# Kernel tuning notes

Hardware: AMD Instinct MI355X
Metric: run time of the kernel (lower is better)

The kernel has to match this reference:

```python
import jax, jax.numpy as jnp
import numpy as np

SCALE = 0.125  # (dim // heads) ** -0.5 = (256 // 4) ** -0.5


def setup_inputs() -> dict:
    key = jax.random.key(0)
    k1, k2, k3, k4, k5 = jax.random.split(key, 5)
    dim, red = 256, 4
    c = dim // red  # 64
    B, H, W = 4, 64, 64
    x = jax.random.normal(k1, (B, dim, H, W), dtype=jnp.float32)
    qkv_w = jax.random.normal(k2, (3 * c, dim), dtype=jnp.float32) * 0.02
    qkv_b = jax.random.normal(k3, (3 * c,), dtype=jnp.float32) * 0.02
    proj_w = jax.random.normal(k4, (dim, c), dtype=jnp.float32) * 0.02
    proj_b = jax.random.normal(k5, (dim,), dtype=jnp.float32) * 0.02
    return {"x": x, "qkv_w": qkv_w, "qkv_b": qkv_b, "proj_w": proj_w, "proj_b": proj_b}


def reference(x, qkv_w, qkv_b, proj_w, proj_b):
    B, C, H, W = x.shape
    # 1x1 conv == channel matmul
    qkv = jnp.einsum('bchw,oc->bohw', x, qkv_w) + qkv_b[None, :, None, None]
    c = qkv.shape[1] // 3
    qkv = qkv.reshape(B, 3 * c, H * W)
    q, k, v = qkv[:, :c], qkv[:, c:2 * c], qkv[:, 2 * c:]  # [B, c, HW]
    # attn[b, n, m] = sum_c q[b,c,n] * k[b,c,m] * scale
    attn = jnp.einsum('bcn,bcm->bnm', q, k) * SCALE
    attn = jax.nn.softmax(attn, axis=-1)  # [B, HW, HW]
    # out[b, c, n] = sum_m v[b,c,m] * attn[b,n,m]   (v @ attn^T)
    out = jnp.einsum('bcm,bnm->bcn', v, attn).reshape(B, c, H, W)
    # proj 1x1 conv back to dim
    return jnp.einsum('bchw,oc->bohw', out, proj_w) + proj_b[None, :, None, None]
```

## Files before the change

kernel.cpp:

```cpp
#include <hip/hip_runtime.h>
#include <hip/hip_bf16.h>


#define N_TOK 4096
#define CDIM  64
#define DIM   256
#define NBAT  4

typedef __attribute__((ext_vector_type(8)))  short          short8;
typedef __attribute__((ext_vector_type(8)))  unsigned short ushort8_t;
typedef __attribute__((ext_vector_type(4)))  unsigned short ushort4_t;
typedef __attribute__((ext_vector_type(4)))  unsigned int   uint4_t;
typedef __attribute__((ext_vector_type(4)))  float          float4_t;
typedef __attribute__((ext_vector_type(16))) float          float16_t;

#if __has_builtin(__builtin_amdgcn_exp2f)
#define QSC  0.18033688011112042f
#define PEXP(x) __builtin_amdgcn_exp2f(x)
#else
#define QSC  0.125f
#define PEXP(x) __expf(x)
#endif

__device__ __forceinline__ unsigned short f2bf(float f) {
  unsigned int u = __builtin_bit_cast(unsigned int, f);
  u += 0x7fffu + ((u >> 16) & 1u);
  return (unsigned short)(u >> 16);
}

__device__ __forceinline__ unsigned int pkcv(float a, float b) {
  __hip_bfloat162 h = __float22bfloat162_rn(make_float2(a, b));
  unsigned int r; __builtin_memcpy(&r, &h, 4); return r;
}

__device__ __forceinline__ short8 ld8(const unsigned short* p) {
  return __builtin_bit_cast(short8, *(const ushort8_t*)p);
}

__device__ __forceinline__ short8 pack8f(float4_t a, float4_t b) {
  uint4_t u;
  u[0] = pkcv(a[0], a[1]); u[1] = pkcv(a[2], a[3]);
  u[2] = pkcv(b[0], b[1]); u[3] = pkcv(b[2], b[3]);
  return __builtin_bit_cast(short8, u);
}

__device__ __forceinline__ float16_t z16() {
  float16_t r;
#pragma unroll
  for (int i = 0; i < 16; ++i) r[i] = 0.0f;
  return r;
}

typedef __attribute__((address_space(1))) const void* gvp;
typedef __attribute__((address_space(3))) void*       lvp;
__device__ __forceinline__ void dma16(const unsigned short* g, unsigned short* l) {
  __builtin_amdgcn_global_load_lds((gvp)g, (lvp)l, 16, 0, 0);
}

#define MFMA(a, b, c) __builtin_amdgcn_mfma_f32_32x32x16_bf16((a), (b), (c), 0, 0, 0)

#define QOFF  0
#define KOFF  1048576
#define VOFF  2097152
#define WQOFF 3145728
#define BSOFF 3194880

__global__ void k_prep(const float* __restrict__ qw, const float* __restrict__ qb,
                       unsigned short* __restrict__ wqs, float* __restrict__ bs)
{
  const int g = blockIdx.x * 256 + threadIdx.x;
  {
    const int lane = g & 63, grp = g >> 6;
    const int w6 = grp >> 4, kk = grp & 15;
    const int o = w6 * 32 + (lane & 31);
    const int c = kk * 16 + (lane >> 5) * 8;
    const float sc = (o < 64) ? QSC : 1.0f;
    const float* src = qw + o * 256 + c;
    ushort8_t u;
#pragma unroll
    for (int j = 0; j < 8; ++j) u[j] = f2bf(src[j] * sc);
    *(ushort8_t*)(wqs + g * 8) = u;
  }
  if (g < 48) {
    float4_t f = *(const float4_t*)(qb + g * 4);
    float4_t o;
#pragma unroll
    for (int j = 0; j < 4; ++j) o[j] = f[j] * ((g * 4 + j) < 64 ? QSC : 1.0f);
    *(float4_t*)(bs + g * 4) = o;
  }
}

#define RS 132

__global__ __launch_bounds__(384, 2) void k_qkv(
    const float* __restrict__ x, const unsigned short* __restrict__ wqs,
    const float* __restrict__ bs, unsigned short* __restrict__ Qf,
    unsigned short* __restrict__ Kf, unsigned short* __restrict__ Vf)
{
  __shared__ unsigned int Xl[64 * RS];
  const int id = blockIdx.x;
  const int b  = (id >> 1) & 3;
  const int nt = (id & 1) | ((id >> 3) << 1);
  const int t  = threadIdx.x;
  const int n0g = nt * 64;

  if (t < 256) {
    const int n0  = (t & 15) * 4;
    const int cpb = t >> 4;
#pragma unroll
    for (int p = 0; p < 8; ++p) {
      const int cp = cpb + 16 * p, c = cp * 2;
      const float* xb = x + (((size_t)(b * DIM + c)) << 12) + n0g + n0;
      float4_t a = *(const float4_t*)xb;
      float4_t d = *(const float4_t*)(xb + 4096);
#pragma unroll
      for (int j = 0; j < 4; ++j)
        Xl[(n0 + j) * RS + cp] = pkcv(a[j], d[j]);
    }
  }
  __syncthreads();

  const int w = t >> 6, lane = t & 63, l31 = lane & 31, lh = lane >> 5;
  const unsigned short* wrow = wqs + ((w * 16) << 9) + lane * 8;
  const unsigned int*   xr0  = &Xl[l31 * RS + lh * 4];
  const unsigned int*   xr1  = &Xl[(32 + l31) * RS + lh * 4];

  float16_t a0 = z16(), a1 = z16();
  if (w < 4) {
#pragma unroll
    for (int kk = 0; kk < 16; ++kk) {
      short8 wf = ld8(wrow + (kk << 9));
      short8 x0 = __builtin_bit_cast(short8, *(const uint4_t*)(xr0 + kk * 8));
      short8 x1 = __builtin_bit_cast(short8, *(const uint4_t*)(xr1 + kk * 8));
      a0 = MFMA(wf, x0, a0);
      a1 = MFMA(wf, x1, a1);
    }
  } else {
#pragma unroll
    for (int kk = 0; kk < 16; ++kk) {
      short8 wf = ld8(wrow + (kk << 9));
      short8 x0 = __builtin_bit_cast(short8, *(const uint4_t*)(xr0 + kk * 8));
      short8 x1 = __builtin_bit_cast(short8, *(const uint4_t*)(xr1 + kk * 8));
      a0 = MFMA(x0, wf, a0);
      a1 = MFMA(x1, wf, a1);
    }
  }

  if (w < 4) {
    unsigned short* dst = (w < 2) ? Qf : Kf;
    const int w2 = w & 1;
#pragma unroll
    for (int sub = 0; sub < 2; ++sub) {
      const float16_t& aa = sub ? a1 : a0;
      const int ch = nt * 2 + sub;
#pragma unroll
      for (int p = 0; p < 4; ++p) {
        const int o = w * 32 + p * 8 + lh * 4;
        float4_t bv = *(const float4_t*)(bs + o);
        ushort4_t pk4;
#pragma unroll
        for (int q = 0; q < 4; ++q) pk4[q] = f2bf(aa[p * 4 + q] + bv[q]);
        const int kkt = w2 * 2 + (p >> 1);
        *(ushort4_t*)(dst + ((((b * 128 + ch) * 4 + kkt) << 9)
                             + (l31 + 32 * (p & 1)) * 8 + lh * 4)) = pk4;
      }
    }
  } else {
    const int ct = w - 4;
    const float bvs = bs[128 + ct * 32 + l31];
#pragma unroll
    for (int sub = 0; sub < 2; ++sub) {
      const float16_t& aa = sub ? a1 : a0;
      const int ch = nt * 2 + sub;
#pragma unroll
      for (int ks = 0; ks < 2; ++ks) {
        ushort8_t pk8;
#pragma unroll
        for (int j = 0; j < 8; ++j) pk8[j] = f2bf(aa[ks * 8 + j] + bvs);
        *(ushort8_t*)(Vf + ((((b * 128 + ch) * 4 + ct * 2 + ks) << 9)
                            + lane * 8)) = pk8;
      }
    }
  }
}

#define OS   68
#define OLS  72
#define NACC (64 * OS + 64)

__global__ __launch_bounds__(512, 1) void k_attn(
    const unsigned short* __restrict__ Qf, const unsigned short* __restrict__ Kf,
    const unsigned short* __restrict__ Vf, const float* __restrict__ pw,
    const float* __restrict__ pb, float* __restrict__ out)
{
  __shared__ __align__(16) unsigned short KV[2][2][16384];
  __shared__ float Oacc[NACC];
  __shared__ __align__(16) unsigned short Ol[64 * OLS];

  const int id = blockIdx.x;
  const int b  = (id >> 1) & 3;
  const int nt = (id & 1) | ((id >> 3) << 1);
  const int t  = threadIdx.x;
  const int wv = t >> 6, lane = t & 63, l31 = lane & 31, lh = lane >> 5;
  const int mq = wv >> 1, nsub = wv & 1;

  for (int i = t; i < NACC; i += 512) Oacc[i] = 0.0f;

  const int kvsel = wv >> 2;
  const int wq2   = (wv & 3) * 2;
  const unsigned short* sg = ((kvsel == 0) ? Kf : Vf)
                             + (((size_t)(b * 128 + wq2)) << 11) + lane * 8;

  short8 qf[4];
#pragma unroll
  for (int kk = 0; kk < 4; ++kk)
    qf[kk] = ld8(Qf + (((b * 128 + nt * 2 + nsub) * 4 + kk) << 9) + lane * 8);

#pragma unroll
  for (int c2 = 0; c2 < 2; ++c2)
#pragma unroll
    for (int kk = 0; kk < 4; ++kk)
      dma16(sg + (c2 << 11) + (kk << 9),
            &KV[0][kvsel][((wq2 + c2) << 11) + (kk << 9)]);

  float16_t oc0 = z16(), oc1 = z16();
  float den = 0.0f;

  __syncthreads();

  for (int t4 = 0; t4 < 16; ++t4) {
    const int cur = t4 & 1;

    if (t4 < 15) {
      const unsigned short* g = sg + (((size_t)(t4 + 1)) << 14);
#pragma unroll
      for (int c2 = 0; c2 < 2; ++c2)
#pragma unroll
        for (int kk = 0; kk < 4; ++kk)
          dma16(g + (c2 << 11) + (kk << 9),
                &KV[cur ^ 1][kvsel][((wq2 + c2) << 11) + (kk << 9)]);
    }

#pragma unroll
    for (int cc = 0; cc < 2; ++cc) {
      const int ch = mq * 2 + cc;
      const unsigned short* kl = &KV[cur][0][ch << 11];
      const unsigned short* vl = &KV[cur][1][ch << 11];

      short8 kf0 = ld8(kl + lane * 8);
      short8 kf1 = ld8(kl + 512 + lane * 8);
      short8 kf2 = ld8(kl + 1024 + lane * 8);
      short8 kf3 = ld8(kl + 1536 + lane * 8);

      float16_t s = z16();
      s = MFMA(kf0, qf[0], s);
      s = MFMA(kf1, qf[1], s);
      s = MFMA(kf2, qf[2], s);
      s = MFMA(kf3, qf[3], s);

      float p[16];
#pragma unroll
      for (int e = 0; e < 16; ++e) p[e] = PEXP(s[e]);
      {
        float d0 = (p[0] + p[1]) + (p[2] + p[3]);
        float d1 = (p[4] + p[5]) + (p[6] + p[7]);
        float d2 = (p[8] + p[9]) + (p[10] + p[11]);
        float d3 = (p[12] + p[13]) + (p[14] + p[15]);
        den += (d0 + d1) + (d2 + d3);
      }

      uint4_t w0, w1;
#pragma unroll
      for (int j = 0; j < 4; ++j) {
        w0[j] = pkcv(p[2 * j], p[2 * j + 1]);
        w1[j] = pkcv(p[8 + 2 * j], p[9 + 2 * j]);
      }
      short8 pf0 = __builtin_bit_cast(short8, w0);
      short8 pf1 = __builtin_bit_cast(short8, w1);

      short8 vf0 = ld8(vl + lane * 8);
      short8 vf1 = ld8(vl + 512 + lane * 8);
      short8 vf2 = ld8(vl + 1024 + lane * 8);
      short8 vf3 = ld8(vl + 1536 + lane * 8);

      oc0 = MFMA(pf0, vf0, oc0);
      oc0 = MFMA(pf1, vf1, oc0);
      oc1 = MFMA(pf0, vf2, oc1);
      oc1 = MFMA(pf1, vf3, oc1);
    }

    __syncthreads();
  }

  den += __shfl_xor(den, 32);

#pragma unroll
  for (int ct = 0; ct < 2; ++ct) {
    const float16_t& oa = ct ? oc1 : oc0;
    const int cc = ct * 32 + l31;
#pragma unroll
    for (int e = 0; e < 16; ++e) {
      const int nr = nsub * 32 + (e & 3) + 8 * (e >> 2) + 4 * lh;
      atomicAdd(&Oacc[nr * OS + cc], oa[e]);
    }
  }
  if (lane < 32) atomicAdd(&Oacc[64 * OS + nsub * 32 + l31], den);
  __syncthreads();

  {
    const int nloc = t >> 3, c8 = (t & 7) * 8;
    float4_t s0 = *(float4_t*)&Oacc[nloc * OS + c8];
    float4_t s1 = *(float4_t*)&Oacc[nloc * OS + c8 + 4];
    const float r = 1.0f / Oacc[64 * OS + nloc];
    uint4_t o4;
    o4[0] = pkcv(s0[0] * r, s0[1] * r);
    o4[1] = pkcv(s0[2] * r, s0[3] * r);
    o4[2] = pkcv(s1[0] * r, s1[1] * r);
    o4[3] = pkcv(s1[2] * r, s1[3] * r);
    *(uint4_t*)&Ol[nloc * OLS + c8] = o4;
  }
  __syncthreads();

  float16_t f0 = z16(), f1 = z16();
  const float* pwrow = pw + (wv * 32 + l31) * 64 + lh * 8;
#pragma unroll
  for (int kk = 0; kk < 4; ++kk) {
    float4_t wa = *(const float4_t*)(pwrow + kk * 16);
    float4_t wb = *(const float4_t*)(pwrow + kk * 16 + 4);
    short8 af = pack8f(wa, wb);
    short8 b0 = ld8(&Ol[l31 * OLS + kk * 16 + lh * 8]);
    short8 b1 = ld8(&Ol[(32 + l31) * OLS + kk * 16 + lh * 8]);
    f0 = MFMA(af, b0, f0);
    f1 = MFMA(af, b1, f1);
  }
  const int n0 = nt * 64;
#pragma unroll
  for (int e = 0; e < 16; ++e) {
    const int o = wv * 32 + (e & 3) + 8 * (e >> 2) + 4 * lh;
    const float bv = pb[o];
    out[((b * 256 + o) << 12) + n0 + l31]      = f0[e] + bv;
    out[((b * 256 + o) << 12) + n0 + 32 + l31] = f1[e] + bv;
  }
}

extern "C" void kernel_launch(void* const* d_in, const int* in_sizes, int n_in,
                              void* d_out, int out_size, void* d_ws, size_t ws_size,
                              hipStream_t stream) {
  const float* x      = (const float*)d_in[0];
  const float* qkv_w  = (const float*)d_in[1];
  const float* qkv_b  = (const float*)d_in[2];
  const float* proj_w = (const float*)d_in[3];
  const float* proj_b = (const float*)d_in[4];
  float* out = (float*)d_out;

  unsigned short* ws  = (unsigned short*)d_ws;
  unsigned short* qf  = ws + QOFF;
  unsigned short* kf  = ws + KOFF;
  unsigned short* vf  = ws + VOFF;
  unsigned short* wqs = ws + WQOFF;
  float*          bs  = (float*)(ws + BSOFF);

  k_prep<<<24, 256, 0, stream>>>(qkv_w, qkv_b, wqs, bs);
  k_qkv<<<256, 384, 0, stream>>>(x, wqs, bs, qf, kf, vf);
  k_attn<<<256, 512, 0, stream>>>(qf, kf, vf, proj_w, proj_b, out);
}
```

Baseline: 133.8 us.

## Load K/V fragments directly from global, drop LDS double buffer and barriers

Each wave now reads its K and V chunk fragments straight from global memory into registers instead of staging them through a double-buffered LDS array with DMA loads and per-iteration __syncthreads. Each wave handles both query subtiles (two sets of Q fragments and accumulators), so K/V fragments are reused across the two query halves in registers. This removes the block-wide barriers and the LDS traffic. In exchange it roughly doubles register pressure and exposes global-load latency, relying on the unroll-by-2 and the cache to hide it.

After: 141.9 us. 1.06x slower.

```diff
diff --git a/kernel.cpp b/kernel.cpp
--- a/kernel.cpp
+++ b/kernel.cpp
@@ -49,12 +49,6 @@
 #pragma unroll
   for (int i = 0; i < 16; ++i) r[i] = 0.0f;
   return r;
-}
-
-typedef __attribute__((address_space(1))) const void* gvp;
-typedef __attribute__((address_space(3))) void*       lvp;
-__device__ __forceinline__ void dma16(const unsigned short* g, unsigned short* l) {
-  __builtin_amdgcn_global_load_lds((gvp)g, (lvp)l, 16, 0, 0);
 }
 
 #define MFMA(a, b, c) __builtin_amdgcn_mfma_f32_32x32x16_bf16((a), (b), (c), 0, 0, 0)
@@ -193,7 +187,6 @@
     const unsigned short* __restrict__ Vf, const float* __restrict__ pw,
     const float* __restrict__ pb, float* __restrict__ out)
 {
-  __shared__ __align__(16) unsigned short KV[2][2][16384];
   __shared__ float Oacc[NACC];
   __shared__ __align__(16) unsigned short Ol[64 * OLS];
 
@@ -202,72 +195,53 @@
   const int nt = (id & 1) | ((id >> 3) << 1);
   const int t  = threadIdx.x;
   const int wv = t >> 6, lane = t & 63, l31 = lane & 31, lh = lane >> 5;
-  const int mq = wv >> 1, nsub = wv & 1;
 
   for (int i = t; i < NACC; i += 512) Oacc[i] = 0.0f;
 
-  const int kvsel = wv >> 2;
-  const int wq2   = (wv & 3) * 2;
-  const unsigned short* sg = ((kvsel == 0) ? Kf : Vf)
-                             + (((size_t)(b * 128 + wq2)) << 11) + lane * 8;
-
-  short8 qf[4];
-#pragma unroll
-  for (int kk = 0; kk < 4; ++kk)
-    qf[kk] = ld8(Qf + (((b * 128 + nt * 2 + nsub) * 4 + kk) << 9) + lane * 8);
-
-#pragma unroll
-  for (int c2 = 0; c2 < 2; ++c2)
-#pragma unroll
-    for (int kk = 0; kk < 4; ++kk)
-      dma16(sg + (c2 << 11) + (kk << 9),
-            &KV[0][kvsel][((wq2 + c2) << 11) + (kk << 9)]);
-
-  float16_t oc0 = z16(), oc1 = z16();
-  float den = 0.0f;
+  short8 qf0[4], qf1[4];
+#pragma unroll
+  for (int kk = 0; kk < 4; ++kk) {
+    qf0[kk] = ld8(Qf + (((b * 128 + nt * 2 + 0) * 4 + kk) << 9) + lane * 8);
+    qf1[kk] = ld8(Qf + (((b * 128 + nt * 2 + 1) * 4 + kk) << 9) + lane * 8);
+  }
+
+  const unsigned short* kb = Kf + (((size_t)(b * 128 + wv)) << 11) + lane * 8;
+  const unsigned short* vb = Vf + (((size_t)(b * 128 + wv)) << 11) + lane * 8;
+
+  float16_t oc00 = z16(), oc01 = z16();
+  float16_t oc10 = z16(), oc11 = z16();
+  float den0 = 0.0f, den1 = 0.0f;
 
   __syncthreads();
 
-  for (int t4 = 0; t4 < 16; ++t4) {
-    const int cur = t4 & 1;
-
-    if (t4 < 15) {
-      const unsigned short* g = sg + (((size_t)(t4 + 1)) << 14);
-#pragma unroll
-      for (int c2 = 0; c2 < 2; ++c2)
-#pragma unroll
-        for (int kk = 0; kk < 4; ++kk)
-          dma16(g + (c2 << 11) + (kk << 9),
-                &KV[cur ^ 1][kvsel][((wq2 + c2) << 11) + (kk << 9)]);
-    }
-
-#pragma unroll
-    for (int cc = 0; cc < 2; ++cc) {
-      const int ch = mq * 2 + cc;
-      const unsigned short* kl = &KV[cur][0][ch << 11];
-      const unsigned short* vl = &KV[cur][1][ch << 11];
-
-      short8 kf0 = ld8(kl + lane * 8);
-      short8 kf1 = ld8(kl + 512 + lane * 8);
-      short8 kf2 = ld8(kl + 1024 + lane * 8);
-      short8 kf3 = ld8(kl + 1536 + lane * 8);
-
-      float16_t s = z16();
-      s = MFMA(kf0, qf[0], s);
-      s = MFMA(kf1, qf[1], s);
-      s = MFMA(kf2, qf[2], s);
-      s = MFMA(kf3, qf[3], s);
-
+#pragma unroll 2
+  for (int it = 0; it < 16; ++it) {
+    const unsigned short* kl = kb + ((size_t)it << 14);
+    const unsigned short* vl = vb + ((size_t)it << 14);
+    short8 kf0 = ld8(kl);
+    short8 kf1 = ld8(kl + 512);
+    short8 kf2 = ld8(kl + 1024);
+    short8 kf3 = ld8(kl + 1536);
+    short8 vf0 = ld8(vl);
+    short8 vf1 = ld8(vl + 512);
+    short8 vf2 = ld8(vl + 1024);
+    short8 vf3 = ld8(vl + 1536);
+
+    float16_t s0 = z16(), s1 = z16();
+    s0 = MFMA(kf0, qf0[0], s0); s0 = MFMA(kf1, qf0[1], s0);
+    s0 = MFMA(kf2, qf0[2], s0); s0 = MFMA(kf3, qf0[3], s0);
+    s1 = MFMA(kf0, qf1[0], s1); s1 = MFMA(kf1, qf1[1], s1);
+    s1 = MFMA(kf2, qf1[2], s1); s1 = MFMA(kf3, qf1[3], s1);
+
+    {
       float p[16];
 #pragma unroll
-      for (int e = 0; e < 16; ++e) p[e] = PEXP(s[e]);
-      {
-        float d0 = (p[0] + p[1]) + (p[2] + p[3]);
-        float d1 = (p[4] + p[5]) + (p[6] + p[7]);
-        float d2 = (p[8] + p[9]) + (p[10] + p[11]);
-        float d3 = (p[12] + p[13]) + (p[14] + p[15]);
-        den += (d0 + d1) + (d2 + d3);
-      }
+      for (int e = 0; e < 16; ++e) p[e] = PEXP(s0[e]);
+      float d0 = (p[0] + p[1]) + (p[2] + p[3]);
+      float d1 = (p[4] + p[5]) + (p[6] + p[7]);
+      float d2 = (p[8] + p[9]) + (p[10] + p[11]);
+      float d3 = (p[12] + p[13]) + (p[14] + p[15]);
+      den0 += (d0 + d1) + (d2 + d3);
 
       uint4_t w0, w1;
 #pragma unroll
@@ -277,34 +251,64 @@
       }
       short8 pf0 = __builtin_bit_cast(short8, w0);
       short8 pf1 = __builtin_bit_cast(short8, w1);
-
-      short8 vf0 = ld8(vl + lane * 8);
-      short8 vf1 = ld8(vl + 512 + lane * 8);
-      short8 vf2 = ld8(vl + 1024 + lane * 8);
-      short8 vf3 = ld8(vl + 1536 + lane * 8);
-
-      oc0 = MFMA(pf0, vf0, oc0);
-      oc0 = MFMA(pf1, vf1, oc0);
-      oc1 = MFMA(pf0, vf2, oc1);
-      oc1 = MFMA(pf1, vf3, oc1);
-    }
-
-    __syncthreads();
-  }
-
-  den += __shfl_xor(den, 32);
+      oc00 = MFMA(pf0, vf0, oc00);
+      oc00 = MFMA(pf1, vf1, oc00);
+      oc01 = MFMA(pf0, vf2, oc01);
+      oc01 = MFMA(pf1, vf3, oc01);
+    }
+
+    {
+      float p[16];
+#pragma unroll
+      for (int e = 0; e < 16; ++e) p[e] = PEXP(s1[e]);
+      float d0 = (p[0] + p[1]) + (p[2] + p[3]);
+      float d1 = (p[4] + p[5]) + (p[6] + p[7]);
+      float d2 = (p[8] + p[9]) + (p[10] + p[11]);
+      float d3 = (p[12] + p[13]) + (p[14] + p[15]);
+      den1 += (d0 + d1) + (d2 + d3);
+
+      uint4_t w0, w1;
+#pragma unroll
+      for (int j = 0; j < 4; ++j) {
+        w0[j] = pkcv(p[2 * j], p[2 * j + 1]);
+        w1[j] = pkcv(p[8 + 2 * j], p[9 + 2 * j]);
+      }
+      short8 pf0 = __builtin_bit_cast(short8, w0);
+      short8 pf1 = __builtin_bit_cast(short8, w1);
+      oc10 = MFMA(pf0, vf0, oc10);
+      oc10 = MFMA(pf1, vf1, oc10);
+      oc11 = MFMA(pf0, vf2, oc11);
+      oc11 = MFMA(pf1, vf3, oc11);
+    }
+  }
+
+  den0 += __shfl_xor(den0, 32);
+  den1 += __shfl_xor(den1, 32);
 
 #pragma unroll
   for (int ct = 0; ct < 2; ++ct) {
-    const float16_t& oa = ct ? oc1 : oc0;
+    const float16_t& oa = ct ? oc01 : oc00;
     const int cc = ct * 32 + l31;
 #pragma unroll
     for (int e = 0; e < 16; ++e) {
-      const int nr = nsub * 32 + (e & 3) + 8 * (e >> 2) + 4 * lh;
+      const int nr = (e & 3) + 8 * (e >> 2) + 4 * lh;
       atomicAdd(&Oacc[nr * OS + cc], oa[e]);
     }
   }
-  if (lane < 32) atomicAdd(&Oacc[64 * OS + nsub * 32 + l31], den);
+#pragma unroll
+  for (int ct = 0; ct < 2; ++ct) {
+    const float16_t& oa = ct ? oc11 : oc10;
+    const int cc = ct * 32 + l31;
+#pragma unroll
+    for (int e = 0; e < 16; ++e) {
+      const int nr = 32 + (e & 3) + 8 * (e >> 2) + 4 * lh;
+      atomicAdd(&Oacc[nr * OS + cc], oa[e]);
+    }
+  }
+  if (lane < 32) {
+    atomicAdd(&Oacc[64 * OS + l31],      den0);
+    atomicAdd(&Oacc[64 * OS + 32 + l31], den1);
+  }
   __syncthreads();
 
   {
```

## Double attention block to 16 waves, one key chunk per wave

Applied to the files above, without the earlier changes.

The attention kernel now launches 1024 threads (16 waves) per block instead of 512. Each wave handles one key/value chunk per stage instead of two, and each wave loads one chunk instead of two. The projection epilogue is split so each wave computes one 32-token half. This gives each CU more waves to hide MFMA and exp latency, at the cost of a lower register budget per thread and more atomic and barrier contention.

After: 151.4 us. 13.2% more time.

```diff
diff --git a/kernel.cpp b/kernel.cpp
--- a/kernel.cpp
+++ b/kernel.cpp
@@ -188,7 +188,7 @@
 #define OLS  72
 #define NACC (64 * OS + 64)
 
-__global__ __launch_bounds__(512, 1) void k_attn(
+__global__ __launch_bounds__(1024, 1) void k_attn(
     const unsigned short* __restrict__ Qf, const unsigned short* __restrict__ Kf,
     const unsigned short* __restrict__ Vf, const float* __restrict__ pw,
     const float* __restrict__ pb, float* __restrict__ out)
@@ -202,14 +202,14 @@
   const int nt = (id & 1) | ((id >> 3) << 1);
   const int t  = threadIdx.x;
   const int wv = t >> 6, lane = t & 63, l31 = lane & 31, lh = lane >> 5;
-  const int mq = wv >> 1, nsub = wv & 1;
-
-  for (int i = t; i < NACC; i += 512) Oacc[i] = 0.0f;
-
-  const int kvsel = wv >> 2;
-  const int wq2   = (wv & 3) * 2;
+  const int ch = wv >> 1, nsub = wv & 1;
+
+  for (int i = t; i < NACC; i += 1024) Oacc[i] = 0.0f;
+
+  const int kvsel = wv >> 3;
+  const int wq    = wv & 7;
   const unsigned short* sg = ((kvsel == 0) ? Kf : Vf)
-                             + (((size_t)(b * 128 + wq2)) << 11) + lane * 8;
+                             + (((size_t)(b * 128 + wq)) << 11) + lane * 8;
 
   short8 qf[4];
 #pragma unroll
@@ -217,11 +217,8 @@
     qf[kk] = ld8(Qf + (((b * 128 + nt * 2 + nsub) * 4 + kk) << 9) + lane * 8);
 
 #pragma unroll
-  for (int c2 = 0; c2 < 2; ++c2)
-#pragma unroll
-    for (int kk = 0; kk < 4; ++kk)
-      dma16(sg + (c2 << 11) + (kk << 9),
-            &KV[0][kvsel][((wq2 + c2) << 11) + (kk << 9)]);
+  for (int kk = 0; kk < 4; ++kk)
+    dma16(sg + (kk << 9), &KV[0][kvsel][(wq << 11) + (kk << 9)]);
 
   float16_t oc0 = z16(), oc1 = z16();
   float den = 0.0f;
@@ -234,60 +231,53 @@
     if (t4 < 15) {
       const unsigned short* g = sg + (((size_t)(t4 + 1)) << 14);
 #pragma unroll
-      for (int c2 = 0; c2 < 2; ++c2)
-#pragma unroll
-        for (int kk = 0; kk < 4; ++kk)
-          dma16(g + (c2 << 11) + (kk << 9),
-                &KV[cur ^ 1][kvsel][((wq2 + c2) << 11) + (kk << 9)]);
-    }
-
-#pragma unroll
-    for (int cc = 0; cc < 2; ++cc) {
-      const int ch = mq * 2 + cc;
-      const unsigned short* kl = &KV[cur][0][ch << 11];
-      const unsigned short* vl = &KV[cur][1][ch << 11];
-
-      short8 kf0 = ld8(kl + lane * 8);
-      short8 kf1 = ld8(kl + 512 + lane * 8);
-      short8 kf2 = ld8(kl + 1024 + lane * 8);
-      short8 kf3 = ld8(kl + 1536 + lane * 8);
-
-      float16_t s = z16();
-      s = MFMA(kf0, qf[0], s);
-      s = MFMA(kf1, qf[1], s);
-      s = MFMA(kf2, qf[2], s);
-      s = MFMA(kf3, qf[3], s);
-
-      float p[16];
-#pragma unroll
-      for (int e = 0; e < 16; ++e) p[e] = PEXP(s[e]);
-      {
-        float d0 = (p[0] + p[1]) + (p[2] + p[3]);
-        float d1 = (p[4] + p[5]) + (p[6] + p[7]);
-        float d2 = (p[8] + p[9]) + (p[10] + p[11]);
-        float d3 = (p[12] + p[13]) + (p[14] + p[15]);
-        den += (d0 + d1) + (d2 + d3);
-      }
-
-      uint4_t w0, w1;
-#pragma unroll
-      for (int j = 0; j < 4; ++j) {
-        w0[j] = pkcv(p[2 * j], p[2 * j + 1]);
-        w1[j] = pkcv(p[8 + 2 * j], p[9 + 2 * j]);
-      }
-      short8 pf0 = __builtin_bit_cast(short8, w0);
-      short8 pf1 = __builtin_bit_cast(short8, w1);
-
-      short8 vf0 = ld8(vl + lane * 8);
-      short8 vf1 = ld8(vl + 512 + lane * 8);
-      short8 vf2 = ld8(vl + 1024 + lane * 8);
-      short8 vf3 = ld8(vl + 1536 + lane * 8);
-
-      oc0 = MFMA(pf0, vf0, oc0);
-      oc0 = MFMA(pf1, vf1, oc0);
-      oc1 = MFMA(pf0, vf2, oc1);
-      oc1 = MFMA(pf1, vf3, oc1);
-    }
+      for (int kk = 0; kk < 4; ++kk)
+        dma16(g + (kk << 9), &KV[cur ^ 1][kvsel][(wq << 11) + (kk << 9)]);
+    }
+
+    const unsigned short* kl = &KV[cur][0][ch << 11];
+    const unsigned short* vl = &KV[cur][1][ch << 11];
+
+    short8 kf0 = ld8(kl + lane * 8);
+    short8 kf1 = ld8(kl + 512 + lane * 8);
+    short8 kf2 = ld8(kl + 1024 + lane * 8);
+    short8 kf3 = ld8(kl + 1536 + lane * 8);
+
+    float16_t s = z16();
+    s = MFMA(kf0, qf[0], s);
+    s = MFMA(kf1, qf[1], s);
+    s = MFMA(kf2, qf[2], s);
+    s = MFMA(kf3, qf[3], s);
+
+    float p[16];
+#pragma unroll
+    for (int e = 0; e < 16; ++e) p[e] = PEXP(s[e]);
+    {
+      float d0 = (p[0] + p[1]) + (p[2] + p[3]);
+      float d1 = (p[4] + p[5]) + (p[6] + p[7]);
+      float d2 = (p[8] + p[9]) + (p[10] + p[11]);
+      float d3 = (p[12] + p[13]) + (p[14] + p[15]);
+      den += (d0 + d1) + (d2 + d3);
+    }
+
+    uint4_t w0, w1;
+#pragma unroll
+    for (int j = 0; j < 4; ++j) {
+      w0[j] = pkcv(p[2 * j], p[2 * j + 1]);
+      w1[j] = pkcv(p[8 + 2 * j], p[9 + 2 * j]);
+    }
+    short8 pf0 = __builtin_bit_cast(short8, w0);
+    short8 pf1 = __builtin_bit_cast(short8, w1);
+
+    short8 vf0 = ld8(vl + lane * 8);
+    short8 vf1 = ld8(vl + 512 + lane * 8);
+    short8 vf2 = ld8(vl + 1024 + lane * 8);
+    short8 vf3 = ld8(vl + 1536 + lane * 8);
+
+    oc0 = MFMA(pf0, vf0, oc0);
+    oc0 = MFMA(pf1, vf1, oc0);
+    oc1 = MFMA(pf0, vf2, oc1);
+    oc1 = MFMA(pf1, vf3, oc1);
 
     __syncthreads();
   }
@@ -307,7 +297,7 @@
   if (lane < 32) atomicAdd(&Oacc[64 * OS + nsub * 32 + l31], den);
   __syncthreads();
 
-  {
+  if (t < 512) {
     const int nloc = t >> 3, c8 = (t & 7) * 8;
     float4_t s0 = *(float4_t*)&Oacc[nloc * OS + c8];
     float4_t s1 = *(float4_t*)&Oacc[nloc * OS + c8 + 4];
@@ -321,25 +311,22 @@
   }
   __syncthreads();
 
-  float16_t f0 = z16(), f1 = z16();
-  const float* pwrow = pw + (wv * 32 + l31) * 64 + lh * 8;
+  float16_t f0 = z16();
+  const float* pwrow = pw + (ch * 32 + l31) * 64 + lh * 8;
 #pragma unroll
   for (int kk = 0; kk < 4; ++kk) {
     float4_t wa = *(const float4_t*)(pwrow + kk * 16);
     float4_t wb = *(const float4_t*)(pwrow + kk * 16 + 4);
     short8 af = pack8f(wa, wb);
-    short8 b0 = ld8(&Ol[l31 * OLS + kk * 16 + lh * 8]);
-    short8 b1 = ld8(&Ol[(32 + l31) * OLS + kk * 16 + lh * 8]);
-    f0 = MFMA(af, b0, f0);
-    f1 = MFMA(af, b1, f1);
+    short8 bfr = ld8(&Ol[(nsub * 32 + l31) * OLS + kk * 16 + lh * 8]);
+    f0 = MFMA(af, bfr, f0);
   }
   const int n0 = nt * 64;
 #pragma unroll
   for (int e = 0; e < 16; ++e) {
-    const int o = wv * 32 + (e & 3) + 8 * (e >> 2) + 4 * lh;
+    const int o = ch * 32 + (e & 3) + 8 * (e >> 2) + 4 * lh;
     const float bv = pb[o];
-    out[((b * 256 + o) << 12) + n0 + l31]      = f0[e] + bv;
-    out[((b * 256 + o) << 12) + n0 + 32 + l31] = f1[e] + bv;
+    out[((b * 256 + o) << 12) + n0 + nsub * 32 + l31] = f0[e] + bv;
   }
 }
 
@@ -362,5 +349,5 @@
 
   k_prep<<<24, 256, 0, stream>>>(qkv_w, qkv_b, wqs, bs);
   k_qkv<<<256, 384, 0, stream>>>(x, wqs, bs, qf, kf, vf);
-  k_attn<<<256, 512, 0, stream>>>(qf, kf, vf, proj_w, proj_b, out);
-}
+  k_attn<<<256, 1024, 0, stream>>>(qf, kf, vf, proj_w, proj_b, out);
+}
```
